# Kernel tuning notes

Measured on AMD Instinct MI355X. Metric: run time of the kernel, lower is better.

Reference implementation:

```python
import jax, jax.numpy as jnp
import numpy as np

B = 32      # graphs per batch
N_NODES = 1024  # nodes per graph
K = 16      # top-k edges per node


def setup_inputs() -> dict:
    key = jax.random.key(0)
    k1, k2 = jax.random.split(key)
    x = jax.random.normal(k1, (B * N_NODES, 128), dtype=jnp.float32) * 0.1
    W = jax.random.normal(k2, (128, 64), dtype=jnp.float32) * (1.0 / np.sqrt(128))
    b = jnp.zeros((64,), dtype=jnp.float32)
    temperature = jnp.asarray(4.0, dtype=jnp.float32)
    return {"x": x, "W": W, "b": b, "temperature": temperature}


def reference(x, W, b, temperature):
    # Encoder: linear node embedding. out: [B*n, C]
    out = x @ W + b
    C = out.shape[-1]
    # Per-graph features, detached as in the original (graph_x = out[...].detach())
    h = jax.lax.stop_gradient(out).reshape(B, N_NODES, C)
    # Pairwise squared euclidean distances per graph: d[b,i,j] = ||h_i - h_j||^2
    sq = jnp.sum(h * h, axis=-1)  # [B, n]
    d_e = sq[:, :, None] + sq[:, None, :] - 2.0 * jnp.einsum('bic,bjc->bij', h, h)
    logits = jnp.exp(-temperature * d_e)  # [B, n, n]
    # Gumbel-noised top-k edge sampling
    z = jax.random.gumbel(jax.random.key(1), logits.shape, logits.dtype)
    _, edges_hat = jax.lax.top_k(logits + z, K)  # [B, n, K] int32
    # Build global edge index with cumulative per-graph node offsets
    offsets = (jnp.arange(B, dtype=jnp.int32) * N_NODES)[:, None, None]  # [B,1,1]
    rows = jnp.broadcast_to(jnp.arange(N_NODES, dtype=jnp.int32)[None, :, None] + offsets,
                            (B, N_NODES, K))
    cols = edges_hat.astype(jnp.int32) + offsets
    edges_idx = jnp.stack((rows.reshape(-1), cols.reshape(-1)))  # [2, B*n*K]
    return out, edges_idx
```

## Files before the change

### kernel.cpp

```cpp
#include <hip/hip_runtime.h>
#include <math.h>

#define OUT_ELEMS 2097152
#define EDGE_ELEMS 524288

__device__ __forceinline__ unsigned int rotl32(unsigned int x, int r){
  return (x << r) | (x >> (32 - r));
}

__device__ __forceinline__ unsigned int tf_bits_part(unsigned int e){
  unsigned int x0 = 0u, x1 = e;
  const unsigned int ks1 = 1u;
  const unsigned int ks2 = 0x1BD11BDBu;
  x1 += ks1;
#define TFR(r) { x0 += x1; x1 = rotl32(x1, r); x1 ^= x0; }
  TFR(13) TFR(15) TFR(26) TFR(6)
  x0 += ks1; x1 += ks2 + 1u;
  TFR(17) TFR(29) TFR(16) TFR(24)
  x0 += ks2; x1 += 0u + 2u;
  TFR(13) TFR(15) TFR(26) TFR(6)
  x0 += 0u;  x1 += ks1 + 3u;
  TFR(17) TFR(29) TFR(16) TFR(24)
  x0 += ks1; x1 += ks2 + 4u;
  TFR(13) TFR(15) TFR(26) TFR(6)
  x0 += ks2; x1 += 0u + 5u;
#undef TFR
  return x0 ^ x1;
}

__device__ __forceinline__ double rcp64(double x){
  double r;
  asm("v_rcp_f64 %0, %1" : "=v"(r) : "v"(x));
  double e = fma(-x, r, 1.0); r = fma(r, e, r);
  e = fma(-x, r, 1.0); r = fma(r, e, r);
  return r;
}

__device__ __forceinline__ double fast_exp(double x){
  double fn = __builtin_rint(x * 1.4426950408889634);
  int n = (int)fn;
  double r = fma(fn, -0.6931471803691238, x);
  r = fma(fn, -1.9082149292705877e-10, r);
  double p = 2.7557319223985893e-06;
  p = fma(r, p, 2.4801587301587302e-05);
  p = fma(r, p, 1.9841269841269841e-04);
  p = fma(r, p, 1.3888888888888889e-03);
  p = fma(r, p, 8.3333333333333333e-03);
  p = fma(r, p, 4.1666666666666664e-02);
  p = fma(r, p, 1.6666666666666666e-01);
  p = fma(r, p, 0.5);
  p = fma(r, p, 1.0);
  p = fma(r, p, 1.0);
  double scale = __longlong_as_double(((long long)(n + 1023)) << 52);
  return p * scale;
}

__device__ __forceinline__ double fast_log(double x){
  long long bx = __double_as_longlong(x);
  long long e = (bx >> 52) - 1023;
  double m = __longlong_as_double((bx & 0xFFFFFFFFFFFFFll) |
                                  0x3FF0000000000000ll);
  int big = m > 1.4142135623730951;
  m = big ? 0.5 * m : m;
  e += big;
  double s = (m - 1.0) * rcp64(m + 1.0);
  double s2 = s * s;
  double p = fma(s2, 2.0/11.0, 2.0/9.0);
  p = fma(s2, p, 2.0/7.0);
  p = fma(s2, p, 2.0/5.0);
  p = fma(s2, p, 2.0/3.0);
  double lm = fma(s * s2, p, 2.0 * s);
  return fma((double)e, 0.6931471805599453, lm);
}

__device__ __forceinline__ float dist2_f32(
    const float* __restrict__ og, const float* __restrict__ hrowf,
    unsigned int jc){
  const float4* cp4 = (const float4*)(og + ((size_t)jc << 6));
  const float4* hp4 = (const float4*)hrowf;
  float a0 = 0.0f, a1 = 0.0f, a2 = 0.0f, a3 = 0.0f;
  #pragma unroll 4
  for (int ch = 0; ch < 16; ++ch){
    float4 cf = cp4[ch];
    float4 hf = hp4[ch];
    float d0 = hf.x - cf.x;
    float d1 = hf.y - cf.y;
    float d2 = hf.z - cf.z;
    float d3 = hf.w - cf.w;
    a0 = fmaf(d0, d0, a0);
    a1 = fmaf(d1, d1, a1);
    a2 = fmaf(d2, d2, a2);
    a3 = fmaf(d3, d3, a3);
  }
  return (a0 + a1) + (a2 + a3);
}

__device__ __forceinline__ unsigned long long pack_key(double sc,
                                                       unsigned int jc){
  unsigned long long kb = (unsigned long long)__double_as_longlong(sc);
  kb ^= (unsigned long long)(((long long)kb) >> 63) | 0x8000000000000000ull;
  return (kb & ~1023ull) | (unsigned long long)(1023u - jc);
}

__device__ __forceinline__ unsigned long long tail64(
    float accf, unsigned int bits, unsigned int jc, double Td, bool act){
  if (!act) return 0ull;
  double sgm = fast_exp(-Td * (double)accf);
  float f = __uint_as_float(0x3f800000u | (bits >> 9)) - 1.0f;
  double u = (f > 0.0f) ? (double)f : 1.1754943508222875e-38;
  double w = -fast_log(u);
  double z = -fast_log(w);
  double sc = sgm + z;
  return pack_key(sc, jc);
}

__device__ __forceinline__ unsigned long long tail32(
    float accf, unsigned int bits, unsigned int jc, float Tf, bool act){
  if (!act) return 0ull;
  float sg = __expf(-Tf * accf);
  float f = __uint_as_float(0x3f800000u | (bits >> 9)) - 1.0f;
  float uf = (f > 0.0f) ? f : 1.17549435e-38f;
  float wv = -__logf(uf);
  float zf = -__logf(wv);
  double sc = (double)sg + (double)zf;
  return pack_key(sc, jc);
}

__device__ __forceinline__ double key_score(unsigned long long k){
  unsigned long long orig = (k >> 63) ? (k ^ 0x8000000000000000ull) : ~k;
  return __longlong_as_double((long long)(orig & ~1023ull));
}

__device__ __forceinline__ unsigned long long bitonic64_desc(
    unsigned long long key, int lane){
  #pragma unroll
  for (int k = 2; k <= 64; k <<= 1){
    #pragma unroll
    for (int j = k >> 1; j; j >>= 1){
      unsigned long long o = __shfl_xor(key, j, 64);
      bool keep_hi = ((lane & k) == 0) == ((lane & j) == 0);
      key = (keep_hi == (o > key)) ? o : key;
    }
  }
  return key;
}

__device__ __forceinline__ unsigned int bitonic32_desc(
    unsigned int key, int lane){
  #pragma unroll
  for (int k = 2; k <= 64; k <<= 1){
    #pragma unroll
    for (int j = k >> 1; j; j >>= 1){
      unsigned int o = __shfl_xor(key, j, 64);
      bool keep_hi = ((lane & k) == 0) == ((lane & j) == 0);
      key = (keep_hi == (o > key)) ? o : key;
    }
  }
  return key;
}

__global__ __launch_bounds__(256) void cvt_wb_v18(
    const float* __restrict__ W, const float* __restrict__ b,
    double* __restrict__ w64, double* __restrict__ b64){
  const int i = blockIdx.x * 256 + threadIdx.x;
  if (i < 8192)      w64[i] = (double)W[i];
  else if (i < 8256) b64[i - 8192] = (double)b[i - 8192];
}

__global__ __launch_bounds__(512) void encoder_v18(
    const float* __restrict__ x, const double* __restrict__ w64,
    const double* __restrict__ b64, float* __restrict__ out){
  __shared__ float xs[64 * 129];
  const int tid = threadIdx.x;

  {
    const float4* xg4 = (const float4*)(x + ((size_t)blockIdx.x << 13));
    #pragma unroll
    for (int s = 0; s < 4; ++s){
      const int idx = tid + (s << 9);
      float4 v = xg4[idx];
      const int r = idx >> 5, k4 = (idx & 31) << 2;
      float* p = &xs[r * 129 + k4];
      p[0] = v.x; p[1] = v.y; p[2] = v.z; p[3] = v.w;
    }
  }
  __syncthreads();

  const int lane = tid & 63;
  const int wu = __builtin_amdgcn_readfirstlane(tid >> 6);
  const int c0 = wu << 3;
  const size_t row = ((size_t)blockIdx.x << 6) + (size_t)lane;

  double acc[8];
  const double* __restrict__ bp = b64 + c0;
  #pragma unroll
  for (int j = 0; j < 8; ++j) acc[j] = bp[j];

  const float* __restrict__ xrow = &xs[lane * 129];
  #pragma unroll 4
  for (int k = 0; k < 128; ++k){
    const double xk = (double)xrow[k];
    const double* __restrict__ wp = w64 + (k << 6) + c0;
    #pragma unroll
    for (int j = 0; j < 8; ++j)
      acc[j] = fma(xk, wp[j], acc[j]);
  }

  float* __restrict__ orow = out + (row << 6) + c0;
  #pragma unroll
  for (int j2 = 0; j2 < 4; ++j2){
    float2 st; st.x = (float)acc[(j2 << 1)]; st.y = (float)acc[(j2 << 1) + 1];
    *(float2*)&orow[j2 << 1] = st;
  }
}

__global__ __launch_bounds__(256, 8) void edges_v18(
    const float* __restrict__ out32, const float* __restrict__ temp,
    float* __restrict__ rows_out, float* __restrict__ cols_out){
  __shared__ float hidf[4][64];
  __shared__ unsigned int cl[4][128];
  const int tid = threadIdx.x, wave = tid >> 6, lane = tid & 63;
  const int gb = blockIdx.x >> 8;
  const int i0 = (blockIdx.x & 255) << 2;
  const int r  = i0 + wave;
  const float* __restrict__ og = out32 + ((size_t)gb << 16);

  hidf[wave][lane] = og[((size_t)r << 6) + lane];

  const unsigned int base = ((unsigned int)gb << 20) | ((unsigned int)r << 10);

  unsigned int v[16];
  unsigned int pmax = 0u;
  #pragma unroll
  for (int m = 0; m < 16; ++m){
    const unsigned int j = (unsigned int)(m << 6) + (unsigned int)lane;
    unsigned int bits = tf_bits_part(base | j);
    v[m] = (bits & ~1023u) | (1023u - j);
    pmax = (v[m] > pmax) ? v[m] : pmax;
  }

  unsigned int sorted = bitonic32_desc(pmax, lane);
  unsigned int b16p = __shfl(sorted, 15, 64);

  float u16 = __uint_as_float(0x3f800000u | (b16p >> 9)) - 1.0f;
  float z16 = -__logf(-__logf(u16));
  float uc  = __expf(-__expf(-(z16 - 1.001f)));
  unsigned int cp = ((__float_as_uint(1.0f + uc) & 0x7FFFFFu) << 9) & ~1023u;

  int cnt = 0;
  #pragma unroll
  for (int m = 0; m < 16; ++m) cnt += (v[m] >= cp) ? 1 : 0;
  int s = cnt;
  #pragma unroll
  for (int off = 1; off < 64; off <<= 1){
    int o = __shfl_up(s, off, 64);
    s += (lane >= off) ? o : 0;
  }
  int nc = __shfl(s, 63, 64);
  nc = (nc > 128) ? 128 : nc;
  int slot = s - cnt;
  #pragma unroll
  for (int m = 0; m < 16; ++m){
    if (v[m] >= cp && slot < 128){
      cl[wave][slot] = 1023u - (v[m] & 1023u);
      ++slot;
    }
  }

  const double Td = (double)temp[0];
  const float  Tf = temp[0];
  unsigned long long key;

  if (nc <= 64){
    const bool act1 = (lane < nc);
    const unsigned int jc1 = act1 ? cl[wave][lane] : 0u;
    const float ac1 = dist2_f32(og, &hidf[wave][0], jc1);
    const unsigned int bt1 = tf_bits_part(base | jc1);
    key = tail32(ac1, bt1, jc1, Tf, act1);
    key = bitonic64_desc(key, lane);
    double s0 = key_score(key);
    unsigned long long kn = __shfl_down(key, 1, 64);
    double s1 = key_score(kn);
    bool tight = (lane < 16) && (key != 0ull) && ((s0 - s1) < 4e-5);
    if (__any(tight)){
      key = tail64(ac1, bt1, jc1, Td, act1);
      key = bitonic64_desc(key, lane);
    }
  } else {
    const bool act1 = (lane < nc);
    const unsigned int jc1 = act1 ? cl[wave][lane] : 0u;
    const float ac1 = dist2_f32(og, &hidf[wave][0], jc1);
    const unsigned int bt1 = tf_bits_part(base | jc1);
    key = tail64(ac1, bt1, jc1, Td, act1);
    key = bitonic64_desc(key, lane);

    const int idx2 = 64 + lane;
    const bool act2 = (idx2 < nc);
    const unsigned int jc2 = act2 ? cl[wave][idx2] : 0u;
    const float ac2 = dist2_f32(og, &hidf[wave][0], jc2);
    const unsigned int bt2 = tf_bits_part(base | jc2);
    unsigned long long k2 = tail64(ac2, bt2, jc2, Td, act2);
    k2 = bitonic64_desc(k2, lane);
    unsigned long long kr = __shfl(k2, 63 - lane, 64);
    key = (kr > key) ? kr : key;
    #pragma unroll
    for (int j2 = 32; j2; j2 >>= 1){
      unsigned long long o = __shfl_xor(key, j2, 64);
      bool left = (lane & j2) == 0;
      bool take = left ? (o > key) : (o < key);
      key = take ? o : key;
    }
  }

  const int grow = (gb << 10) + r;
  if (lane < 16){
    rows_out[((size_t)grow << 4) + lane] = (float)grow;
    cols_out[((size_t)grow << 4) + lane] =
        (float)((gb << 10) + (1023 - (int)(key & 1023ull)));
  }
}

extern "C" void kernel_launch(void* const* d_in, const int* in_sizes, int n_in,
                              void* d_out, int out_size, void* d_ws, size_t ws_size,
                              hipStream_t stream){
  const float* x = (const float*)d_in[0];
  const float* W = (const float*)d_in[1];
  const float* b = (const float*)d_in[2];
  const float* T = (const float*)d_in[3];
  float* out      = (float*)d_out;
  float* rows_out = out + OUT_ELEMS;
  float* cols_out = rows_out + EDGE_ELEMS;

  double* w64 = (double*)d_ws;
  double* b64 = w64 + 8192;

  cvt_wb_v18<<<33, 256, 0, stream>>>(W, b, w64, b64);
  encoder_v18<<<512, 512, 0, stream>>>(x, w64, b64, out);
  edges_v18<<<8192, 256, 0, stream>>>(out, T, rows_out, cols_out);
}
```

Baseline: 177.1 us.

## Fold weight conversion into encoder and remap threads to rows-by-column layout

Removes the separate kernel that converted W and b to double in the workspace, cutting one launch and a dependency. The encoder now has each lane own one output column and each wave own 8 rows. Each W element is read as a coalesced fp32 global load and converted in registers, and x is staged in shared memory as double so the row values are LDS broadcasts. Stores become coalesced per row. The trade-off is double the shared memory (64KB) for the x tile, which can lower occupancy, plus 128 extra converts per thread.

```diff
diff --git a/kernel.cpp b/kernel.cpp
--- a/kernel.cpp
+++ b/kernel.cpp
@@ -159,62 +159,52 @@
   return key;
 }
 
-__global__ __launch_bounds__(256) void cvt_wb_v18(
-    const float* __restrict__ W, const float* __restrict__ b,
-    double* __restrict__ w64, double* __restrict__ b64){
-  const int i = blockIdx.x * 256 + threadIdx.x;
-  if (i < 8192)      w64[i] = (double)W[i];
-  else if (i < 8256) b64[i - 8192] = (double)b[i - 8192];
-}
-
-__global__ __launch_bounds__(512) void encoder_v18(
-    const float* __restrict__ x, const double* __restrict__ w64,
-    const double* __restrict__ b64, float* __restrict__ out){
-  __shared__ float xs[64 * 129];
+__global__ __launch_bounds__(512) void encoder_v21(
+    const float* __restrict__ x, const float* __restrict__ W,
+    const float* __restrict__ b, float* __restrict__ out){
+  __shared__ double x64[8192];
   const int tid = threadIdx.x;
+  const size_t r0 = (size_t)blockIdx.x << 6;
 
   {
-    const float4* xg4 = (const float4*)(x + ((size_t)blockIdx.x << 13));
+    const float4* xg4 = (const float4*)(x + (r0 << 7));
     #pragma unroll
     for (int s = 0; s < 4; ++s){
       const int idx = tid + (s << 9);
       float4 v = xg4[idx];
-      const int r = idx >> 5, k4 = (idx & 31) << 2;
-      float* p = &xs[r * 129 + k4];
-      p[0] = v.x; p[1] = v.y; p[2] = v.z; p[3] = v.w;
+      const int e0 = idx << 2;
+      x64[e0 + 0] = (double)v.x;
+      x64[e0 + 1] = (double)v.y;
+      x64[e0 + 2] = (double)v.z;
+      x64[e0 + 3] = (double)v.w;
     }
   }
   __syncthreads();
 
   const int lane = tid & 63;
-  const int wu = __builtin_amdgcn_readfirstlane(tid >> 6);
-  const int c0 = wu << 3;
-  const size_t row = ((size_t)blockIdx.x << 6) + (size_t)lane;
-
+  const int wv = tid >> 6;
+  const int rw = wv << 3;
+
+  const double bc = (double)b[lane];
   double acc[8];
-  const double* __restrict__ bp = b64 + c0;
-  #pragma unroll
-  for (int j = 0; j < 8; ++j) acc[j] = bp[j];
-
-  const float* __restrict__ xrow = &xs[lane * 129];
+  #pragma unroll
+  for (int i = 0; i < 8; ++i) acc[i] = bc;
+
+  const double* __restrict__ xp0 = &x64[rw << 7];
   #pragma unroll 4
   for (int k = 0; k < 128; ++k){
-    const double xk = (double)xrow[k];
-    const double* __restrict__ wp = w64 + (k << 6) + c0;
-    #pragma unroll
-    for (int j = 0; j < 8; ++j)
-      acc[j] = fma(xk, wp[j], acc[j]);
-  }
-
-  float* __restrict__ orow = out + (row << 6) + c0;
-  #pragma unroll
-  for (int j2 = 0; j2 < 4; ++j2){
-    float2 st; st.x = (float)acc[(j2 << 1)]; st.y = (float)acc[(j2 << 1) + 1];
-    *(float2*)&orow[j2 << 1] = st;
-  }
-}
-
-__global__ __launch_bounds__(256, 8) void edges_v18(
+    const double wkc = (double)W[(k << 6) + lane];
+    #pragma unroll
+    for (int i = 0; i < 8; ++i)
+      acc[i] = fma(xp0[(i << 7) + k], wkc, acc[i]);
+  }
+
+  #pragma unroll
+  for (int i = 0; i < 8; ++i)
+    out[((r0 + (size_t)(rw + i)) << 6) + lane] = (float)acc[i];
+}
+
+__global__ __launch_bounds__(256, 8) void edges_v21(
     const float* __restrict__ out32, const float* __restrict__ temp,
     float* __restrict__ rows_out, float* __restrict__ cols_out){
   __shared__ float hidf[4][64];
@@ -331,10 +321,6 @@
   float* rows_out = out + OUT_ELEMS;
   float* cols_out = rows_out + EDGE_ELEMS;
 
-  double* w64 = (double*)d_ws;
-  double* b64 = w64 + 8192;
-
-  cvt_wb_v18<<<33, 256, 0, stream>>>(W, b, w64, b64);
-  encoder_v18<<<512, 512, 0, stream>>>(x, w64, b64, out);
-  edges_v18<<<8192, 256, 0, stream>>>(out, T, rows_out, cols_out);
-}
+  encoder_v21<<<512, 512, 0, stream>>>(x, W, b, out);
+  edges_v21<<<8192, 256, 0, stream>>>(out, T, rows_out, cols_out);
+}
```

Result: no change. 180.0 us (+1.7%).
